# Kernel tuning notes

Hardware: AMD Instinct MI355X
Metric: run time of the kernel (lower is better)

The kernel has to match this reference:

```python
import jax, jax.numpy as jnp
import numpy as np
from jax import lax

WS = 32          # region_size
N = WS * WS      # tokens per region = 1024
H = 8            # num_heads
HD = 64          # head_dim
C = H * HD       # dim = 512
B = 8            # num_regions * batch
K = 15           # conv_k
SCALE = HD ** -0.5


def _rel_index():
    # Swin relative position index, computed statically with numpy.
    coords = np.stack(np.meshgrid(np.arange(WS), np.arange(WS), indexing='ij'))  # [2,WS,WS]
    flat = coords.reshape(2, -1)                                                 # [2,N]
    rel = (flat[:, :, None] - flat[:, None, :]).transpose(1, 2, 0)               # [N,N,2]
    rel = rel.copy()
    rel[..., 0] += WS - 1
    rel[..., 1] += WS - 1
    rel[..., 0] *= 2 * WS - 1
    return rel.sum(-1)  # [N,N] int

_REL_IDX = jnp.asarray(_rel_index())


def setup_inputs() -> dict:
    key = jax.random.key(0)
    ks = jax.random.split(key, 6)
    return {
        'x': jax.random.normal(ks[0], (B, N, C), dtype=jnp.float32),
        'w_qkv': jax.random.normal(ks[1], (3 * C, C), dtype=jnp.float32) * 0.02,
        'b_qkv': jnp.zeros((3 * C,), dtype=jnp.float32),
        'w_proj': jax.random.normal(ks[2], (C, C), dtype=jnp.float32) * 0.02,
        'b_proj': jnp.zeros((C,), dtype=jnp.float32),
        'rel_table': jax.random.normal(ks[3], ((2 * WS - 1) ** 2, H), dtype=jnp.float32) * 0.02,
        'pe_w': jax.random.normal(ks[4], (H, 1, K, 1), dtype=jnp.float32) * 0.02,
        'pe_b': jnp.zeros((H,), dtype=jnp.float32),
    }


def reference(x, w_qkv, b_qkv, w_proj, b_proj, rel_table, pe_w, pe_b):
    b, n, c = x.shape
    qkv = (x @ w_qkv.T + b_qkv).reshape(b, n, 3, H, HD)
    q = jnp.moveaxis(qkv[:, :, 0], 2, 1)  # [B,H,N,HD]
    k = jnp.moveaxis(qkv[:, :, 1], 2, 1)
    v = jnp.moveaxis(qkv[:, :, 2], 2, 1)

    attn = jnp.einsum('bhnd,bhmd->bhnm', q * SCALE, k)  # [B,H,N,N]

    # depthwise (per-head) conv over the query axis of the attention matrix, kernel (K,1)
    pe = lax.conv_general_dilated(
        attn, pe_w, window_strides=(1, 1), padding=[(K // 2, K // 2), (0, 0)],
        dimension_numbers=('NCHW', 'OIHW', 'NCHW'), feature_group_count=H,
    ) + pe_b[None, :, None, None]
    attn = attn + pe

    # relative position bias gather: [N*N] -> [N,N,H] -> [H,N,N]
    bias = rel_table[_REL_IDX.reshape(-1)].reshape(n, n, H).transpose(2, 0, 1)
    attn = jax.nn.softmax(attn + bias[None], axis=-1)

    out = jnp.einsum('bhnm,bhmd->bnhd', attn, v).reshape(b, n, c)
    return out @ w_proj.T + b_proj
```

## Files before the change

kernel.cpp:

```cpp
#include <hip/hip_runtime.h>

typedef __bf16 bf16x8 __attribute__((ext_vector_type(8)));
typedef float f32x4 __attribute__((ext_vector_type(4)));
typedef unsigned short u16;
typedef unsigned int u32;
typedef unsigned long long u64;

__device__ __forceinline__ float bf2f(u16 x){ u32 u = ((u32)x)<<16; return __builtin_bit_cast(float,u); }
__device__ __forceinline__ u16 f2bf(float f){ u32 u = __builtin_bit_cast(u32,f); u = (u + 0x7fffu + ((u>>16)&1u)) >> 16; return (u16)u; }

__device__ __forceinline__ void glds16(const u16* g, u16* l){
  __builtin_amdgcn_global_load_lds((const __attribute__((address_space(1))) u32*)g,
                                   (__attribute__((address_space(3))) u32*)l, 16, 0, 0);
}

static constexpr float L2E = 1.4426950408889634f;
static constexpr float QSC = 0.125f * 1.4426950408889634f;

__global__ void k_cvtall(const float* __restrict__ x, const float* __restrict__ wq,
                         const float* __restrict__ wp, const float* __restrict__ rt,
                         u16* __restrict__ xo, u16* __restrict__ wqo,
                         u16* __restrict__ wpo, u64* __restrict__ rel2){
  int bid = blockIdx.x;
  if (bid < 5120){
    int i = bid*256 + threadIdx.x;
    const float* s; u16* d; int base;
    if (i < 1048576){ s=x; d=xo; base=0; }
    else if (i < 1245184){ s=wq; d=wqo; base=1048576; }
    else { s=wp; d=wpo; base=1245184; }
    int j = i - base;
    float4 v = reinterpret_cast<const float4*>(s)[j];
    reinterpret_cast<ushort4*>(d)[j] = make_ushort4(f2bf(v.x),f2bf(v.y),f2bf(v.z),f2bf(v.w));
  } else {
    int i = (bid-5120)*256 + threadIdx.x;
    if (i < 31752){
      int h = i / 3969, i2 = i - h*3969;
      u64 v = 0;
      #pragma unroll
      for (int j=0;j<4;j++){
        int idx = i2-3+j;
        u16 bb = 0;
        if (idx >= 0) bb = f2bf(rt[idx*8+h]*L2E);
        v |= (u64)bb << (16*j);
      }
      rel2[i] = v;
    }
  }
}

__device__ __forceinline__ void acc8(float* acc, uint4 v, float w){
  acc[0]=fmaf(w, bf2f((u16)(v.x)),     acc[0]); acc[1]=fmaf(w, bf2f((u16)(v.x>>16)), acc[1]);
  acc[2]=fmaf(w, bf2f((u16)(v.y)),     acc[2]); acc[3]=fmaf(w, bf2f((u16)(v.y>>16)), acc[3]);
  acc[4]=fmaf(w, bf2f((u16)(v.z)),     acc[4]); acc[5]=fmaf(w, bf2f((u16)(v.z>>16)), acc[5]);
  acc[6]=fmaf(w, bf2f((u16)(v.w)),     acc[6]); acc[7]=fmaf(w, bf2f((u16)(v.w>>16)), acc[7]);
}
__global__ void k_qconv(const u16* __restrict__ q, u16* __restrict__ qp, const float* __restrict__ pw){
  int idx = blockIdx.x*256 + threadIdx.x;
  int dc = idx&7, n = (idx>>3)&1023, bh = idx>>13, h = bh&7;
  const u16* base = q + (long)bh*65536 + dc*8;
  float wgt[15];
  #pragma unroll
  for (int t=0;t<15;t++) wgt[t] = pw[h*15+t];
  float acc[8];
  {
    uint4 cv = *reinterpret_cast<const uint4*>(base + n*64);
    acc[0]=bf2f((u16)cv.x); acc[1]=bf2f((u16)(cv.x>>16));
    acc[2]=bf2f((u16)cv.y); acc[3]=bf2f((u16)(cv.y>>16));
    acc[4]=bf2f((u16)cv.z); acc[5]=bf2f((u16)(cv.z>>16));
    acc[6]=bf2f((u16)cv.w); acc[7]=bf2f((u16)(cv.w>>16));
  }
  #pragma unroll
  for (int t=0;t<15;t++){
    int nn = n - 7 + t;
    if (nn >= 0 && nn < 1024){
      uint4 v = *reinterpret_cast<const uint4*>(base + nn*64);
      acc8(acc, v, wgt[t]);
    }
  }
  u16* out = qp + (long)bh*65536 + n*64 + dc*8;
  *reinterpret_cast<ushort4*>(out)   = make_ushort4(f2bf(acc[0]),f2bf(acc[1]),f2bf(acc[2]),f2bf(acc[3]));
  *reinterpret_cast<ushort4*>(out+4) = make_ushort4(f2bf(acc[4]),f2bf(acc[5]),f2bf(acc[6]),f2bf(acc[7]));
}

template<int MODE>
__global__ __launch_bounds__(256) void k_gemm(
  const u16* __restrict__ A, const u16* __restrict__ Bw, const float* __restrict__ bias,
  u16* __restrict__ qo, u16* __restrict__ ko, u16* __restrict__ vo, float* __restrict__ co)
{
  constexpr int K = 512;
  constexpr int NX = (MODE==0) ? 12 : 4;
  constexpr int CPX = NX*64/8;
  __shared__ __align__(16) u16 lA[3][4096];
  __shared__ __align__(16) u16 lB[3][4096];
  const int lin = blockIdx.y*NX + blockIdx.x;
  const int swz = (lin&7)*CPX + (lin>>3);
  const int i0 = (swz/NX)*128, j0 = (swz%NX)*128;
  const int T = threadIdx.x;
  const int w = T>>6, lane = T&63, g = lane>>4, cl = lane&15;
  const int wr = (w>>1)*64, wc = (w&1)*64;
  const int sr = T>>2, sk = 8*(T&3);
  f32x4 acc[4][4];
  #pragma unroll
  for (int a=0;a<4;a++)
    #pragma unroll
    for (int b=0;b<4;b++) acc[a][b] = (f32x4){0.f,0.f,0.f,0.f};

  auto STAGE = [&](int t, u16* bA, u16* bB){
    glds16(A  + (long)(i0+sr)*K    + t*32 + sk, bA + 8*T);
    glds16(A  + (long)(i0+64+sr)*K + t*32 + sk, bA + 2048 + 8*T);
    glds16(Bw + (long)(j0+sr)*K    + t*32 + sk, bB + 8*T);
    glds16(Bw + (long)(j0+64+sr)*K + t*32 + sk, bB + 2048 + 8*T);
  };
  STAGE(0, lA[0], lB[0]);
  STAGE(1, lA[1], lB[1]);
  int cur = 0, sb = 2;
  for (int t=0;t<16;t++){
    if (t<15) asm volatile("s_waitcnt vmcnt(4)" ::: "memory");
    else      asm volatile("s_waitcnt vmcnt(0)" ::: "memory");
    __builtin_amdgcn_s_barrier();
    asm volatile("" ::: "memory");
    if (t<14) STAGE(t+2, lA[sb], lB[sb]);
    const u16* cA = lA[cur];
    const u16* cB = lB[cur];
    bf16x8 af[4], bfr[4];
    #pragma unroll
    for (int mf=0;mf<4;mf++) af[mf]  = *reinterpret_cast<const bf16x8*>(cA + (wr+16*mf+cl)*32 + 8*g);
    #pragma unroll
    for (int nf=0;nf<4;nf++) bfr[nf] = *reinterpret_cast<const bf16x8*>(cB + (wc+16*nf+cl)*32 + 8*g);
    __builtin_amdgcn_s_setprio(1);
    #pragma unroll
    for (int mf=0;mf<4;mf++)
      #pragma unroll
      for (int nf=0;nf<4;nf++)
        acc[mf][nf] = __builtin_amdgcn_mfma_f32_16x16x32_bf16(af[mf], bfr[nf], acc[mf][nf], 0,0,0);
    __builtin_amdgcn_s_setprio(0);
    cur = (cur==2)?0:cur+1;
    sb  = (sb==2)?0:sb+1;
  }

  #pragma unroll
  for (int mf=0;mf<4;mf++){
    #pragma unroll
    for (int nf=0;nf<4;nf++){
      const int col = j0 + wc + 16*nf + cl;
      const float bb = bias[col];
      const int row0 = i0 + wr + 16*mf + 4*g;
      if (MODE==0){
        const int part = col>>9, h=(col>>6)&7, dd=col&63;
        const int b = row0>>10, n0 = row0&1023, bh = b*8+h;
        if (part==2){
          const int a32 = n0 & ~31, G = (n0>>2)&7;
          const int stb = ((G&3)<<3) | ((G>>2)<<2);
          ushort4 pk = make_ushort4(f2bf(acc[mf][nf][0]+bb), f2bf(acc[mf][nf][1]+bb),
                                    f2bf(acc[mf][nf][2]+bb), f2bf(acc[mf][nf][3]+bb));
          *reinterpret_cast<ushort4*>(vo + ((long)bh*64+dd)*1024 + a32 + stb) = pk;
        } else {
          #pragma unroll
          for (int e=0;e<4;e++){
            float v = acc[mf][nf][e] + bb;
            if (part==0) qo[((long)bh*1024+n0+e)*64+dd] = f2bf(v*QSC);
            else         ko[((long)bh*1024+n0+e)*64+dd] = f2bf(v);
          }
        }
      } else {
        #pragma unroll
        for (int e=0;e<4;e++)
          co[(long)(row0+e)*512 + col] = acc[mf][nf][e] + bb;
      }
    }
  }
}

__global__ __launch_bounds__(256,2) void k_attn(
  const u16* __restrict__ Qp, const u16* __restrict__ Kb, const u16* __restrict__ VT,
  const u64* __restrict__ relT2, u16* __restrict__ Ao)
{
  __shared__ __align__(16) u16 kls[4][4096];
  __shared__ __align__(16) u16 vls[4][4096];
  const int bid = blockIdx.x;
  const int xcd = bid&7, slot = bid>>3;
  const int bh = xcd*8 + (slot>>3), rb = slot&7;
  const int b = bh>>3, h = bh&7;
  const int T = threadIdx.x, w=T>>6, lane=T&63, g=lane>>4, cl=lane&15;
  const int rowbase = rb*128 + w*32;
  const int qr[2] = { rowbase + cl, rowbase + 16 + cl };
  bf16x8 qf[2][2];
  #pragma unroll
  for (int G=0;G<2;G++){
    const u16* Qr = Qp + ((long)bh*1024 + qr[G])*64;
    qf[G][0] = *reinterpret_cast<const bf16x8*>(Qr + 8*g);
    qf[G][1] = *reinterpret_cast<const bf16x8*>(Qr + 32 + 8*g);
  }
  const int rt[2] = { (qr[0]>>5)*63 + (qr[0]&31) + 1984,
                      (qr[1]>>5)*63 + (qr[1]&31) + 1984 };
  const u64* relTh = relT2 + h*3969;
  const u16* Kbh = Kb + (long)bh*65536;
  const u16* Vbh = VT + (long)bh*65536;
  float lsum[2] = {0.f, 0.f};
  f32x4 oacc[2][4];
  #pragma unroll
  for (int G=0;G<2;G++)
    #pragma unroll
    for (int c=0;c<4;c++) oacc[G][c] = (f32x4){0.f,0.f,0.f,0.f};

  auto STAGE = [&](int m0, int bi){
    #pragma unroll
    for (int s=0;s<2;s++){
      int idx = s*256 + T, row = idx>>3, u = idx&7, sw = (u ^ (row&7))<<3;
      glds16(Kbh + (m0+row)*64 + sw,         kls[bi] + idx*8);
      glds16(Vbh + (long)row*1024 + m0 + sw, vls[bi] + idx*8);
    }
  };
  STAGE(0,0); STAGE(64,1); STAGE(128,2);

  for (int t=0;t<16;t++){
    const int m0 = t<<6;
    u64 rx[2][4];
    #pragma unroll
    for (int G=0;G<2;G++)
      #pragma unroll
      for (int c=0;c<4;c++){
        const int kk = m0 + 16*c + 4*g;
        rx[G][c] = relTh[rt[G] - ((kk>>5)*63 + (kk&31))];
      }
    if (t<=13)      asm volatile("s_waitcnt vmcnt(16)" ::: "memory");
    else if (t==14) asm volatile("s_waitcnt vmcnt(12)" ::: "memory");
    else            asm volatile("s_waitcnt vmcnt(8)"  ::: "memory");
    __builtin_amdgcn_s_barrier();
    asm volatile("" ::: "memory");
    if (t<13) STAGE(m0+192, (t+3)&3);

    const char* kb = (const char*)kls[t&3];
    const char* vb = (const char*)vls[t&3];
    f32x4 sacc[2][4];
    #pragma unroll
    for (int G=0;G<2;G++)
      #pragma unroll
      for (int c=0;c<4;c++) sacc[G][c] = (f32x4){0.f,0.f,0.f,0.f};
    __builtin_amdgcn_s_setprio(1);
    #pragma unroll
    for (int c=0;c<4;c++){
      const int r = 16*c + cl, rs = r&7;
      const char* kr = kb + r*128;
      bf16x8 kf0 = *reinterpret_cast<const bf16x8*>(kr + ((g    ^rs)<<4));
      bf16x8 kf1 = *reinterpret_cast<const bf16x8*>(kr + (((4+g)^rs)<<4));
      #pragma unroll
      for (int G=0;G<2;G++){
        sacc[G][c] = __builtin_amdgcn_mfma_f32_16x16x32_bf16(kf0, qf[G][0], sacc[G][c],0,0,0);
        sacc[G][c] = __builtin_amdgcn_mfma_f32_16x16x32_bf16(kf1, qf[G][1], sacc[G][c],0,0,0);
      }
    }
    __builtin_amdgcn_s_setprio(0);
    float p[2][4][4];
    #pragma unroll
    for (int G=0;G<2;G++)
      #pragma unroll
      for (int c=0;c<4;c++)
        #pragma unroll
        for (int e=0;e<4;e++){
          float bias = __builtin_bit_cast(float, ((u32)((u16)(rx[G][c] >> (16*(3-e)))))<<16);
          p[G][c][e] = __builtin_amdgcn_exp2f(sacc[G][c][e] + bias);
        }
    #pragma unroll
    for (int G=0;G<2;G++)
      #pragma unroll
      for (int c=0;c<4;c++) lsum[G] += (p[G][c][0]+p[G][c][1]) + (p[G][c][2]+p[G][c][3]);
    bf16x8 pa[2][2];
    #pragma unroll
    for (int G=0;G<2;G++)
      #pragma unroll
      for (int e=0;e<4;e++){
        pa[G][0][e]   = (__bf16)p[G][0][e];  pa[G][0][4+e] = (__bf16)p[G][1][e];
        pa[G][1][e]   = (__bf16)p[G][2][e];  pa[G][1][4+e] = (__bf16)p[G][3][e];
      }
    __builtin_amdgcn_s_setprio(1);
    #pragma unroll
    for (int ks=0;ks<2;ks++)
      #pragma unroll
      for (int c2=0;c2<4;c2++){
        const int dd = 16*c2 + cl, dsw = dd&7;
        bf16x8 vf = *reinterpret_cast<const bf16x8*>(vb + dd*128 + (((4*ks+g)^dsw)<<4));
        #pragma unroll
        for (int G=0;G<2;G++)
          oacc[G][c2] = __builtin_amdgcn_mfma_f32_16x16x32_bf16(pa[G][ks], vf, oacc[G][c2],0,0,0);
      }
    __builtin_amdgcn_s_setprio(0);
  }
  #pragma unroll
  for (int G=0;G<2;G++){
    lsum[G] += __shfl_xor(lsum[G], 16, 64);
    lsum[G] += __shfl_xor(lsum[G], 32, 64);
  }
  #pragma unroll
  for (int G=0;G<2;G++)
    #pragma unroll
    for (int e=0;e<4;e++){
      float inv = 1.0f/__shfl(lsum[G], 4*g+e, 64);
      const long orow = (long)b*1024 + rowbase + 16*G + 4*g + e;
      #pragma unroll
      for (int c2=0;c2<4;c2++)
        Ao[orow*512 + h*64 + 16*c2 + cl] = f2bf(oacc[G][c2][e]*inv);
    }
}

extern "C" void kernel_launch(void* const* d_in, const int* in_sizes, int n_in,
                              void* d_out, int out_size, void* d_ws, size_t ws_size,
                              hipStream_t stream)
{
  const float* x         = (const float*)d_in[0];
  const float* w_qkv     = (const float*)d_in[1];
  const float* b_qkv     = (const float*)d_in[2];
  const float* w_proj    = (const float*)d_in[3];
  const float* b_proj    = (const float*)d_in[4];
  const float* rel_table = (const float*)d_in[5];
  const float* pe_w      = (const float*)d_in[6];
  (void)in_sizes; (void)n_in; (void)out_size; (void)ws_size;

  u16* ws    = (u16*)d_ws;
  u16* x_bf  = ws;
  u16* wq_bf = x_bf  + 4194304;
  u16* wp_bf = wq_bf + 786432;
  u16* q_bf  = wp_bf + 262144;
  u16* k_bf  = q_bf  + 4194304;
  u16* vt_bf = k_bf  + 4194304;
  u16* qp_bf = vt_bf + 4194304;
  u16* ao_bf = qp_bf + 4194304;
  u64* relT2 = (u64*)(ao_bf + 4194304);

  k_cvtall<<<5245,256,0,stream>>>(x, w_qkv, w_proj, rel_table, x_bf, wq_bf, wp_bf, relT2);
  k_gemm<0><<<dim3(12,64),256,0,stream>>>(x_bf, wq_bf, b_qkv, q_bf, k_bf, vt_bf, nullptr);
  k_qconv<<<2048,256,0,stream>>>(q_bf, qp_bf, pe_w);
  k_attn<<<512,256,0,stream>>>(qp_bf, k_bf, vt_bf, relT2, ao_bf);
  k_gemm<1><<<dim3(4,64),256,0,stream>>>(ao_bf, wp_bf, b_proj, nullptr, nullptr, nullptr, (float*)d_out);
}
```

Baseline: 84.18 us.

## Software-pipeline attention QK with softmax/PV and shrink proj GEMM tile

The attention loop is restructured into a two-stage ping-pong: the QK MFMAs for tile t run alongside the softmax and PV work for tile t-1, using two score and bias register sets. This lets matrix and exp/VALU work overlap. The proj GEMM (MODE 1) now uses 64-row tiles with 4 warps across columns, doubling the grid to 512 blocks for better CU occupancy. Bias unpacking is also simplified with mask and shift instead of per-element shifts. The costs are higher register pressure in the attention kernel and a more intricate vmcnt/barrier schedule.

```diff
diff --git a/kernel.cpp b/kernel.cpp
--- a/kernel.cpp
+++ b/kernel.cpp
@@ -88,26 +88,29 @@
   u16* __restrict__ qo, u16* __restrict__ ko, u16* __restrict__ vo, float* __restrict__ co)
 {
   constexpr int K = 512;
+  constexpr int BM = (MODE==0) ? 128 : 64;
   constexpr int NX = (MODE==0) ? 12 : 4;
-  constexpr int CPX = NX*64/8;
-  __shared__ __align__(16) u16 lA[3][4096];
+  constexpr int CPX = NX*(8192/BM)/8;
+  constexpr int NF = (MODE==0) ? 4 : 2;
+  __shared__ __align__(16) u16 lA[3][BM*32];
   __shared__ __align__(16) u16 lB[3][4096];
   const int lin = blockIdx.y*NX + blockIdx.x;
   const int swz = (lin&7)*CPX + (lin>>3);
-  const int i0 = (swz/NX)*128, j0 = (swz%NX)*128;
+  const int i0 = (swz/NX)*BM, j0 = (swz%NX)*128;
   const int T = threadIdx.x;
   const int w = T>>6, lane = T&63, g = lane>>4, cl = lane&15;
-  const int wr = (w>>1)*64, wc = (w&1)*64;
+  const int wr = (MODE==0) ? (w>>1)*64 : 0;
+  const int wc = (MODE==0) ? (w&1)*64 : w*32;
   const int sr = T>>2, sk = 8*(T&3);
-  f32x4 acc[4][4];
+  f32x4 acc[4][NF];
   #pragma unroll
   for (int a=0;a<4;a++)
     #pragma unroll
-    for (int b=0;b<4;b++) acc[a][b] = (f32x4){0.f,0.f,0.f,0.f};
+    for (int b=0;b<NF;b++) acc[a][b] = (f32x4){0.f,0.f,0.f,0.f};
 
   auto STAGE = [&](int t, u16* bA, u16* bB){
     glds16(A  + (long)(i0+sr)*K    + t*32 + sk, bA + 8*T);
-    glds16(A  + (long)(i0+64+sr)*K + t*32 + sk, bA + 2048 + 8*T);
+    if (MODE==0) glds16(A + (long)(i0+64+sr)*K + t*32 + sk, bA + 2048 + 8*T);
     glds16(Bw + (long)(j0+sr)*K    + t*32 + sk, bB + 8*T);
     glds16(Bw + (long)(j0+64+sr)*K + t*32 + sk, bB + 2048 + 8*T);
   };
@@ -115,23 +118,27 @@
   STAGE(1, lA[1], lB[1]);
   int cur = 0, sb = 2;
   for (int t=0;t<16;t++){
-    if (t<15) asm volatile("s_waitcnt vmcnt(4)" ::: "memory");
-    else      asm volatile("s_waitcnt vmcnt(0)" ::: "memory");
+    if (t<15){
+      if (MODE==0) asm volatile("s_waitcnt vmcnt(4)" ::: "memory");
+      else         asm volatile("s_waitcnt vmcnt(3)" ::: "memory");
+    } else {
+      asm volatile("s_waitcnt vmcnt(0)" ::: "memory");
+    }
     __builtin_amdgcn_s_barrier();
     asm volatile("" ::: "memory");
     if (t<14) STAGE(t+2, lA[sb], lB[sb]);
     const u16* cA = lA[cur];
     const u16* cB = lB[cur];
-    bf16x8 af[4], bfr[4];
+    bf16x8 af[4], bfr[NF];
     #pragma unroll
     for (int mf=0;mf<4;mf++) af[mf]  = *reinterpret_cast<const bf16x8*>(cA + (wr+16*mf+cl)*32 + 8*g);
     #pragma unroll
-    for (int nf=0;nf<4;nf++) bfr[nf] = *reinterpret_cast<const bf16x8*>(cB + (wc+16*nf+cl)*32 + 8*g);
+    for (int nf=0;nf<NF;nf++) bfr[nf] = *reinterpret_cast<const bf16x8*>(cB + (wc+16*nf+cl)*32 + 8*g);
     __builtin_amdgcn_s_setprio(1);
     #pragma unroll
     for (int mf=0;mf<4;mf++)
       #pragma unroll
-      for (int nf=0;nf<4;nf++)
+      for (int nf=0;nf<NF;nf++)
         acc[mf][nf] = __builtin_amdgcn_mfma_f32_16x16x32_bf16(af[mf], bfr[nf], acc[mf][nf], 0,0,0);
     __builtin_amdgcn_s_setprio(0);
     cur = (cur==2)?0:cur+1;
@@ -141,7 +148,7 @@
   #pragma unroll
   for (int mf=0;mf<4;mf++){
     #pragma unroll
-    for (int nf=0;nf<4;nf++){
+    for (int nf=0;nf<NF;nf++){
       const int col = j0 + wc + 16*nf + cl;
       const float bb = bias[col];
       const int row0 = i0 + wr + 16*mf + 4*g;
@@ -183,16 +190,18 @@
   const int b = bh>>3, h = bh&7;
   const int T = threadIdx.x, w=T>>6, lane=T&63, g=lane>>4, cl=lane&15;
   const int rowbase = rb*128 + w*32;
-  const int qr[2] = { rowbase + cl, rowbase + 16 + cl };
+  const int qr0 = rowbase + cl, qr1 = rowbase + 16 + cl;
   bf16x8 qf[2][2];
-  #pragma unroll
-  for (int G=0;G<2;G++){
-    const u16* Qr = Qp + ((long)bh*1024 + qr[G])*64;
-    qf[G][0] = *reinterpret_cast<const bf16x8*>(Qr + 8*g);
-    qf[G][1] = *reinterpret_cast<const bf16x8*>(Qr + 32 + 8*g);
-  }
-  const int rt[2] = { (qr[0]>>5)*63 + (qr[0]&31) + 1984,
-                      (qr[1]>>5)*63 + (qr[1]&31) + 1984 };
+  {
+    const u16* Qr0 = Qp + ((long)bh*1024 + qr0)*64;
+    const u16* Qr1 = Qp + ((long)bh*1024 + qr1)*64;
+    qf[0][0] = *reinterpret_cast<const bf16x8*>(Qr0 + 8*g);
+    qf[0][1] = *reinterpret_cast<const bf16x8*>(Qr0 + 32 + 8*g);
+    qf[1][0] = *reinterpret_cast<const bf16x8*>(Qr1 + 8*g);
+    qf[1][1] = *reinterpret_cast<const bf16x8*>(Qr1 + 32 + 8*g);
+  }
+  const int rt[2] = { (qr0>>5)*63 + (qr0&31) + 1984,
+                      (qr1>>5)*63 + (qr1&31) + 1984 };
   const u64* relTh = relT2 + h*3969;
   const u16* Kbh = Kb + (long)bh*65536;
   const u16* Vbh = VT + (long)bh*65536;
@@ -211,28 +220,7 @@
       glds16(Vbh + (long)row*1024 + m0 + sw, vls[bi] + idx*8);
     }
   };
-  STAGE(0,0); STAGE(64,1); STAGE(128,2);
-
-  for (int t=0;t<16;t++){
-    const int m0 = t<<6;
-    u64 rx[2][4];
-    #pragma unroll
-    for (int G=0;G<2;G++)
-      #pragma unroll
-      for (int c=0;c<4;c++){
-        const int kk = m0 + 16*c + 4*g;
-        rx[G][c] = relTh[rt[G] - ((kk>>5)*63 + (kk&31))];
-      }
-    if (t<=13)      asm volatile("s_waitcnt vmcnt(16)" ::: "memory");
-    else if (t==14) asm volatile("s_waitcnt vmcnt(12)" ::: "memory");
-    else            asm volatile("s_waitcnt vmcnt(8)"  ::: "memory");
-    __builtin_amdgcn_s_barrier();
-    asm volatile("" ::: "memory");
-    if (t<13) STAGE(m0+192, (t+3)&3);
-
-    const char* kb = (const char*)kls[t&3];
-    const char* vb = (const char*)vls[t&3];
-    f32x4 sacc[2][4];
+  auto QK = [&](const char* kb, f32x4 (&sacc)[2][4]){
     #pragma unroll
     for (int G=0;G<2;G++)
       #pragma unroll
@@ -251,16 +239,32 @@
       }
     }
     __builtin_amdgcn_s_setprio(0);
+  };
+  auto RELLOAD = [&](int t, u64 (&rx)[2][4]){
+    #pragma unroll
+    for (int G=0;G<2;G++)
+      #pragma unroll
+      for (int c=0;c<4;c++){
+        const int kk = (t<<6) + 16*c + 4*g;
+        rx[G][c] = relTh[rt[G] - ((kk>>5)*63 + (kk&31))];
+      }
+  };
+  auto SMPV = [&](const char* vb, f32x4 (&sacc)[2][4], u64 (&rx)[2][4]){
     float p[2][4][4];
     #pragma unroll
     for (int G=0;G<2;G++)
       #pragma unroll
-      for (int c=0;c<4;c++)
-        #pragma unroll
-        for (int e=0;e<4;e++){
-          float bias = __builtin_bit_cast(float, ((u32)((u16)(rx[G][c] >> (16*(3-e)))))<<16);
-          p[G][c][e] = __builtin_amdgcn_exp2f(sacc[G][c][e] + bias);
-        }
+      for (int c=0;c<4;c++){
+        const u32 lo = (u32)rx[G][c], hi = (u32)(rx[G][c]>>32);
+        const float b0 = __builtin_bit_cast(float, hi & 0xffff0000u);
+        const float b1 = __builtin_bit_cast(float, hi << 16);
+        const float b2 = __builtin_bit_cast(float, lo & 0xffff0000u);
+        const float b3 = __builtin_bit_cast(float, lo << 16);
+        p[G][c][0] = __builtin_amdgcn_exp2f(sacc[G][c][0] + b0);
+        p[G][c][1] = __builtin_amdgcn_exp2f(sacc[G][c][1] + b1);
+        p[G][c][2] = __builtin_amdgcn_exp2f(sacc[G][c][2] + b2);
+        p[G][c][3] = __builtin_amdgcn_exp2f(sacc[G][c][3] + b3);
+      }
     #pragma unroll
     for (int G=0;G<2;G++)
       #pragma unroll
@@ -285,7 +289,44 @@
           oacc[G][c2] = __builtin_amdgcn_mfma_f32_16x16x32_bf16(pa[G][ks], vf, oacc[G][c2],0,0,0);
       }
     __builtin_amdgcn_s_setprio(0);
-  }
+  };
+
+  f32x4 saccA[2][4], saccB[2][4];
+  u64 rxA[2][4], rxB[2][4];
+
+  STAGE(0,0); STAGE(64,1);
+  asm volatile("s_waitcnt vmcnt(4)" ::: "memory");
+  __builtin_amdgcn_s_barrier();
+  asm volatile("" ::: "memory");
+
+  for (int tp=0; tp<7; ++tp){
+    const int t0 = 2*tp, t1 = t0+1;
+    QK((const char*)kls[t0&3], saccA);
+    RELLOAD(t0, rxA);
+    if (tp>0) SMPV((const char*)vls[(t0-1)&3], saccB, rxB);
+    STAGE((t0+2)<<6, (t0+2)&3);
+    asm volatile("s_waitcnt vmcnt(12)" ::: "memory");
+    __builtin_amdgcn_s_barrier();
+    asm volatile("" ::: "memory");
+    QK((const char*)kls[t1&3], saccB);
+    RELLOAD(t1, rxB);
+    SMPV((const char*)vls[t0&3], saccA, rxA);
+    STAGE((t1+2)<<6, (t1+2)&3);
+    asm volatile("s_waitcnt vmcnt(12)" ::: "memory");
+    __builtin_amdgcn_s_barrier();
+    asm volatile("" ::: "memory");
+  }
+  QK((const char*)kls[2], saccA);
+  RELLOAD(14, rxA);
+  SMPV((const char*)vls[1], saccB, rxB);
+  asm volatile("s_waitcnt vmcnt(8)" ::: "memory");
+  __builtin_amdgcn_s_barrier();
+  asm volatile("" ::: "memory");
+  QK((const char*)kls[3], saccB);
+  RELLOAD(15, rxB);
+  SMPV((const char*)vls[2], saccA, rxA);
+  SMPV((const char*)vls[3], saccB, rxB);
+
   #pragma unroll
   for (int G=0;G<2;G++){
     lsum[G] += __shfl_xor(lsum[G], 16, 64);
@@ -331,5 +372,5 @@
   k_gemm<0><<<dim3(12,64),256,0,stream>>>(x_bf, wq_bf, b_qkv, q_bf, k_bf, vt_bf, nullptr);
   k_qconv<<<2048,256,0,stream>>>(q_bf, qp_bf, pe_w);
   k_attn<<<512,256,0,stream>>>(qp_bf, k_bf, vt_bf, relT2, ao_bf);
-  k_gemm<1><<<dim3(4,64),256,0,stream>>>(ao_bf, wp_bf, b_proj, nullptr, nullptr, nullptr, (float*)d_out);
-}
+  k_gemm<1><<<dim3(4,128),256,0,stream>>>(ao_bf, wp_bf, b_proj, nullptr, nullptr, nullptr, (float*)d_out);
+}
```

New measurement: 82.57 us. About the same (-1.9%).
